# Kernel optimization log

Hardware: AMD Instinct MI355X
Metric: run time of the kernel (lower is better)

The kernel has to match this reference:

```python
import jax, jax.numpy as jnp
import numpy as np

DIM, NH, NKV, HD = 1024, 16, 16, 64
ROPE_BASE, TRAIN_LEN, YARN_MAX = 10000.0, 1024, 4096
GROUP = 64
EPS = 1e-05


def ternary_ste(w):
    # bf16 group-wise ternary quantization with straight-through estimator
    wb = w.astype(jnp.bfloat16)
    wg = wb.reshape(-1, GROUP)
    scale = jnp.clip(jnp.mean(jnp.abs(wg), axis=-1, keepdims=True), 1e-08, None)
    q = jnp.clip(jnp.round(wg / scale), -1, 1)
    deq = (q * scale).reshape(wb.shape)
    return wb + jax.lax.stop_gradient(deq - wb)


def rmsnorm(x):
    return x * jax.lax.rsqrt(jnp.mean(x * x, axis=-1, keepdims=True) + EPS)


def rope_tables(seqlen, dtype):
    rd = HD  # rope_dims=0 -> full head_dim
    ar = np.arange(0, rd, 2, dtype=np.float32)
    inv_freq = 1.0 / ROPE_BASE ** (ar / rd)
    scale = TRAIN_LEN / YARN_MAX
    ramp = np.clip((ar / rd - 0.25) / 0.75, 0.0, 1.0)
    inv_freq = inv_freq / (ramp * (1.0 / scale - 1.0) + 1.0)
    freqs = np.arange(seqlen, dtype=np.float32)[:, None] * inv_freq[None, :]
    cos = jnp.asarray(np.cos(freqs), dtype)[None, :, None, :]  # [1,S,1,HD/2]
    sin = jnp.asarray(np.sin(freqs), dtype)[None, :, None, :]
    return cos, sin


def apply_rotary(x, cos, sin):
    half = x.shape[-1] // 2
    x1, x2 = x[..., :half], x[..., half:]
    return jnp.concatenate([x1 * cos + x2 * sin, -x1 * sin + x2 * cos], axis=-1)


def causal_attn(q, k, v):
    # q,k,v: [B,S,H,d]; softmax scale 1/sqrt(d)
    d = q.shape[-1]
    S = q.shape[1]
    s = jnp.einsum('bqhd,bkhd->bhqk', q, k) * (1.0 / jnp.sqrt(jnp.asarray(d, q.dtype)))
    mask = jnp.tril(jnp.ones((S, S), bool))
    s = jnp.where(mask[None, None], s, -jnp.inf)
    p = jax.nn.softmax(s, axis=-1)
    return jnp.einsum('bhqk,bkhd->bqhd', p, v)


def tversky_proj(x, features, prototypes, theta, alpha, beta):
    # x: [B,S,D] -> [B,S,D]
    x_f = jnp.einsum('bsd,fd->bsf', x, features)          # [B,S,16]
    p_f = ternary_ste(prototypes).astype(features.dtype) @ features.T  # [D,16]
    x_s = jax.nn.sigmoid(x_f * 5.0)
    p_s = jax.nn.sigmoid(p_f * 5.0)
    x_a = x_f * x_s
    p_a = p_f * p_s
    return (jnp.abs(theta) * jnp.einsum('bsf,of->bso', x_a, p_a)
            - jnp.abs(alpha) * jnp.einsum('bsf,of->bso', x_a, 1.0 - p_s)
            - jnp.abs(beta) * jnp.einsum('bsf,of->bso', 1.0 - x_s, p_a))


def setup_inputs() -> dict:
    key = jax.random.key(0)
    ks = jax.random.split(key, 8)
    B, S = 2, 2048
    x = jax.random.normal(ks[0], (B, S, DIM), jnp.float32)
    w_qkv = jax.random.normal(ks[1], (NH * HD + 2 * NKV * HD, DIM), jnp.float32) * 0.02
    features = jax.random.uniform(ks[2], (16, DIM), jnp.float32, -0.02, 0.02)
    prototypes = jax.random.uniform(ks[3], (DIM, DIM), jnp.float32, -0.02, 0.02)
    theta = jnp.asarray(1.0, jnp.float32)
    alpha = jnp.asarray(0.5, jnp.float32)
    beta = jnp.asarray(0.5, jnp.float32)
    q_gain = jnp.full((NH,), 1.0, jnp.float32)
    diff_lambda = jnp.full((NH,), 0.5, jnp.float32)
    return {"x": x, "w_qkv": w_qkv, "features": features, "prototypes": prototypes,
            "theta": theta, "alpha": alpha, "beta": beta,
            "q_gain": q_gain, "diff_lambda": diff_lambda}


def reference(x, w_qkv, features, prototypes, theta, alpha, beta, q_gain, diff_lambda):
    B, S, D = x.shape
    w_t = ternary_ste(w_qkv).astype(x.dtype)
    qkv = x @ w_t.T
    q_out = qkv[..., :NH * HD]
    k_out = qkv[..., NH * HD:NH * HD + NKV * HD]
    v_out = qkv[..., NH * HD + NKV * HD:]
    q = rmsnorm(q_out.reshape(B, S, NH, HD))
    k = rmsnorm(k_out.reshape(B, S, NKV, HD))
    v = v_out.reshape(B, S, NKV, HD)
    cos, sin = rope_tables(S, q.dtype)
    q = apply_rotary(q, cos, sin)
    k = apply_rotary(k, cos, sin)
    q = q * q_gain.astype(q.dtype)[None, None, :, None]
    half = HD // 2
    y1 = causal_attn(q[..., :half], k[..., :half], v[..., :half])
    y2 = causal_attn(q[..., half:], k[..., half:], v[..., half:])
    lam = diff_lambda.astype(y1.dtype)[None, None, :, None]
    y = jnp.concatenate([y1 - lam * y2, y1 + lam * y2], axis=-1).reshape(B, S, D)
    return tversky_proj(y, features, prototypes, theta, alpha, beta)
```

## Files before the change

### kernel.cpp

```cpp
#include <hip/hip_runtime.h>
#include <hip/hip_bf16.h>
#include <math.h>

#define DIM   1024
#define NHEAD 16
#define SLEN  2048
#define BATCH 2
#define NROWS (BATCH*SLEN)
#define QKV_N 3072

typedef __attribute__((ext_vector_type(8))) short short8v;
typedef __attribute__((ext_vector_type(4))) short short4v;
typedef __attribute__((ext_vector_type(4))) float f32x4;
typedef __attribute__((ext_vector_type(4))) unsigned int u32x4;

__device__ __forceinline__ unsigned short rne16(float f) {
  unsigned u = __float_as_uint(f);
  u += 0x7FFFu + ((u >> 16) & 1u);
  return (unsigned short)(u >> 16);
}
__device__ __forceinline__ float rnef(float f) {
  unsigned u = __float_as_uint(f);
  u += 0x7FFFu + ((u >> 16) & 1u);
  return __uint_as_float(u & 0xFFFF0000u);
}
__device__ __forceinline__ unsigned pk2(float a, float b) {
  unsigned r;
  asm("v_cvt_pk_bf16_f32 %0, %1, %2" : "=v"(r) : "v"(a), "v"(b));
  return r;
}

__device__ __forceinline__ void gld16(const unsigned short* g, unsigned short* l) {
  __builtin_amdgcn_global_load_lds(
      (const __attribute__((address_space(1))) unsigned int*)g,
      (__attribute__((address_space(3))) unsigned int*)l, 16, 0, 0);
}

__global__ void __launch_bounds__(256) k_prep(
    const float* __restrict__ w_qkv, const float* __restrict__ protos,
    const float* __restrict__ x, const float* __restrict__ F,
    unsigned short* __restrict__ Wb, float* __restrict__ PT,
    unsigned short* __restrict__ Xhi, unsigned short* __restrict__ Xlo,
    float* __restrict__ cosT, float* __restrict__ sinT,
    float* __restrict__ FS, float* __restrict__ FD) {
  const int blk = blockIdx.x, tid = threadIdx.x;
  if (blk < 4096) {
    const bool isw = (blk < 3072);
    const int idx = (isw ? blk * 256 + tid : (blk - 3072) * 256 + tid) * 4;
    const float* src = isw ? w_qkv : protos;
    float4 v = *(const float4*)(src + idx);
    float b0 = rnef(v.x), b1 = rnef(v.y), b2 = rnef(v.z), b3 = rnef(v.w);
    float a0 = fabsf(b0), a1 = fabsf(b1), a2 = fabsf(b2), a3 = fabsf(b3);
    #pragma unroll
    for (int off = 8; off >= 1; off >>= 1) {
      a0 += __shfl_xor(a0, off); a1 += __shfl_xor(a1, off);
      a2 += __shfl_xor(a2, off); a3 += __shfl_xor(a3, off);
    }
    float s = (a0 + a2) + (a1 + a3);
    float scale = fmaxf(rnef(s * (1.0f / 64.0f)), 1e-8f);
    auto tern = [&](float wb) -> float {
      float q = fminf(1.0f, fmaxf(-1.0f, rintf(rnef(wb / scale))));
      float deq = rnef(q * scale);
      float d = rnef(deq - wb);
      return wb + d;
    };
    if (isw) {
      short4v o;
      o[0] = (short)rne16(tern(b0)); o[1] = (short)rne16(tern(b1));
      o[2] = (short)rne16(tern(b2)); o[3] = (short)rne16(tern(b3));
      *(short4v*)(Wb + idx) = o;
    } else {
      float4 o = {rnef(tern(b0)), rnef(tern(b1)), rnef(tern(b2)), rnef(tern(b3))};
      *(float4*)(PT + idx) = o;
    }
  } else if (blk < 8192) {
    int idx = (blk - 4096) * 256 + tid;
    float4 v = *(const float4*)(x + (size_t)idx * 4);
    short4v hi, lo;
    float h0 = rnef(v.x); hi[0] = (short)rne16(v.x); lo[0] = (short)rne16(v.x - h0);
    float h1 = rnef(v.y); hi[1] = (short)rne16(v.y); lo[1] = (short)rne16(v.y - h1);
    float h2 = rnef(v.z); hi[2] = (short)rne16(v.z); lo[2] = (short)rne16(v.z - h2);
    float h3 = rnef(v.w); hi[3] = (short)rne16(v.w); lo[3] = (short)rne16(v.w - h3);
    *(short4v*)(Xhi + (size_t)idx * 4) = hi;
    *(short4v*)(Xlo + (size_t)idx * 4) = lo;
  } else if (blk < 8448) {
    int idx = (blk - 8192) * 256 + tid;
    int s = idx >> 5, j = idx & 31;
    double inv  = 1.0 / pow(10000.0, (double)(2 * j) / 64.0);
    double ramp = ((double)(2 * j) / 64.0 - 0.25) / 0.75;
    ramp = ramp < 0.0 ? 0.0 : (ramp > 1.0 ? 1.0 : ramp);
    inv /= (ramp * 3.0 + 1.0);
    float freq = (float)s * (float)inv;
    cosT[idx] = (float)cos((double)freq);
    sinT[idx] = (float)sin((double)freq);
  } else {
    int idx = (blk - 8448) * 256 + tid;
    int f = idx >> 9, hd = idx & 511;
    int h = hd >> 5, d = hd & 31;
    float a = F[f * 1024 + h * 64 + d];
    float b = F[f * 1024 + h * 64 + 32 + d];
    FS[idx] = a + b;
    FD[idx] = b - a;
  }
}

#define FEN() asm volatile("" ::: "memory")
#define SB()  do { FEN(); __builtin_amdgcn_s_barrier(); FEN(); } while (0)
#define WL()  do { asm volatile("s_waitcnt lgkmcnt(0)" ::: "memory"); \
                   __builtin_amdgcn_sched_barrier(0); } while (0)
#define WVN(n) asm volatile("s_waitcnt vmcnt(" #n ")" ::: "memory")

__global__ void __launch_bounds__(512, 2) k_gemm4(
    const unsigned short* __restrict__ Xhi, const unsigned short* __restrict__ Xlo,
    const unsigned short* __restrict__ Wb, float* __restrict__ C) {
  __shared__ unsigned char lds[114688];
  const int t = threadIdx.x;
  const int lane = t & 63;
  const int qL = lane & 15, quad = lane >> 4;
  const int wid = t >> 6;
  const int wm = wid >> 2, wn = wid & 3;
  const int bid = blockIdx.x;
  const int swz = (bid & 7) * 32 + (bid >> 3);
  const int by = swz >> 4, bx = swz & 15;
  const int bm = by * 256, bn = bx * 192;
  const int inner = qL * 64 + ((quad * 16) ^ ((qL & 8) << 2));
  int rj[3], cj[3];
  #pragma unroll
  for (int j = 0; j < 3; ++j) {
    int L = j * 8192 + t * 16;
    int Lp = L ^ (((L >> 9) & 1) << 5);
    int st = Lp >> 10;
    rj[j] = (st >> 1) * 16 + ((Lp >> 6) & 15);
    cj[j] = (st & 1) * 32 + ((Lp & 63) >> 1);
  }
  unsigned char* AHI = lds;
  unsigned char* ALO = lds + 32768;
  unsigned char* BB  = lds + 65536;

  auto STA = [&](const unsigned short* __restrict__ pan, unsigned char* reg,
                 int kc, int h) {
    unsigned char* lb = reg + h * 16384 + (t >> 6) * 1024;
    #pragma unroll
    for (int j = 0; j < 2; ++j) {
      int rr = bm + ((rj[j] >> 6) * 128) + h * 64 + (rj[j] & 63);
      gld16(pan + (size_t)rr * 1024 + kc + cj[j], (unsigned short*)(lb + j * 8192));
    }
  };
  auto STB = [&](int kc, int buf) {
    unsigned char* lb = BB + buf * 24576 + (t >> 6) * 1024;
    #pragma unroll
    for (int j = 0; j < 3; ++j)
      gld16(Wb + (size_t)(bn + rj[j]) * 1024 + kc + cj[j],
            (unsigned short*)(lb + j * 8192));
  };

  short8v aF[4][2], bF[3][2];
  f32x4 acc[2][4][3];
  const f32x4 zz = {0.f, 0.f, 0.f, 0.f};
  #pragma unroll
  for (int q_ = 0; q_ < 2; ++q_)
    #pragma unroll
    for (int m_ = 0; m_ < 4; ++m_)
      #pragma unroll
      for (int n_ = 0; n_ < 3; ++n_) acc[q_][m_][n_] = zz;

  auto RA = [&](unsigned char* reg, int qm_) {
    #pragma unroll
    for (int mi = 0; mi < 4; ++mi)
      #pragma unroll
      for (int ks = 0; ks < 2; ++ks)
        aF[mi][ks] = *(const short8v*)(reg + qm_ * 16384 +
                                       ((((wm * 4 + mi) << 1) + ks) << 10) + inner);
  };
  auto RB = [&](int buf) {
    #pragma unroll
    for (int ni = 0; ni < 3; ++ni)
      #pragma unroll
      for (int ks = 0; ks < 2; ++ks)
        bF[ni][ks] = *(const short8v*)(BB + buf * 24576 +
                                       ((((wn * 3 + ni) << 1) + ks) << 10) + inner);
  };
  auto MM = [&](int qm_) {
    __builtin_amdgcn_s_setprio(1);
    #pragma unroll
    for (int ks = 0; ks < 2; ++ks)
      #pragma unroll
      for (int mi = 0; mi < 4; ++mi)
        #pragma unroll
        for (int ni = 0; ni < 3; ++ni)
          acc[qm_][mi][ni] = __builtin_amdgcn_mfma_f32_16x16x32_bf16(
              aF[mi][ks], bF[ni][ks], acc[qm_][mi][ni], 0, 0, 0);
    __builtin_amdgcn_s_setprio(0);
  };

  STB(0, 0); STA(Xhi, AHI, 0, 0); STA(Xhi, AHI, 0, 1); STA(Xlo, ALO, 0, 0);
  WVN(4);
  SB();

  #pragma unroll 1
  for (int i = 0; i < 16; ++i) {
    const int kc = i * 64, kn = kc + 64;
    const bool nl = (i < 15);
    const int cb = i & 1, nb = cb ^ 1;
    RA(AHI, 0); RB(cb); STA(Xlo, ALO, kc, 1);
    SB(); WL(); MM(0);
    WVN(4);
    SB();
    RA(AHI, 1);
    if (nl) { STB(kn, nb); STA(Xhi, AHI, kn, 0); }
    SB(); WL(); MM(1);
    if (nl) { WVN(7); } else { WVN(2); }
    SB();
    RA(ALO, 0);
    if (nl) STA(Xhi, AHI, kn, 1);
    SB(); WL(); MM(0);
    if (nl) { WVN(7); } else { WVN(0); }
    SB();
    RA(ALO, 1);
    if (nl) STA(Xlo, ALO, kn, 0);
    SB(); WL(); MM(1);
    if (nl) WVN(4);
    SB();
  }

  #pragma unroll
  for (int qm_ = 0; qm_ < 2; ++qm_)
    #pragma unroll
    for (int mi = 0; mi < 4; ++mi) {
      const int row0 = bm + wm * 128 + qm_ * 64 + mi * 16 + quad * 4;
      #pragma unroll
      for (int ni = 0; ni < 3; ++ni) {
        const int col = bn + wn * 48 + ni * 16 + qL;
        #pragma unroll
        for (int r = 0; r < 4; ++r)
          C[(size_t)(row0 + r) * QKV_N + col] = acc[qm_][mi][ni][r];
      }
    }
}

__device__ __forceinline__ float dot4(float4 a, float4 b) {
  return fmaf(a.x, b.x, fmaf(a.y, b.y, fmaf(a.z, b.z, a.w * b.w)));
}
__global__ void __launch_bounds__(256) k_mid(const float* __restrict__ QKV,
    const float* __restrict__ cosT, const float* __restrict__ sinT,
    const float* __restrict__ q_gain,
    unsigned short* __restrict__ QB16, unsigned short* __restrict__ KB16,
    unsigned short* __restrict__ VT16,
    const float* __restrict__ PT, const float* __restrict__ F,
    const float* __restrict__ thp, const float* __restrict__ alp,
    const float* __restrict__ bep,
    float* __restrict__ A1T, float* __restrict__ A2T) {
  __shared__ short Vt[64][34];
  const int blk = blockIdx.x, t = threadIdx.x;
  if (blk < 8192) {
    int gid = blk * 256 + t;
    int l = gid & 63;
    int w = gid >> 6;
    int r = w >> 3;
    int u = (w & 7) * 4 + (l >> 4);
    int isk = u >> 4, h = u & 15;
    int d0 = (l & 15) * 4;
    float4 xv = *(const float4*)(QKV + (size_t)r * 3072 + isk * 1024 + h * 64 + d0);
    float s0 = xv.x * xv.x, s1 = xv.y * xv.y;
    float s2 = xv.z * xv.z, s3 = xv.w * xv.w;
    #pragma unroll
    for (int off = 8; off >= 1; off >>= 1) {
      s0 += __shfl_xor(s0, off); s1 += __shfl_xor(s1, off);
      s2 += __shfl_xor(s2, off); s3 += __shfl_xor(s3, off);
    }
    float ss = (s0 + s2) + (s1 + s3);
    float inv = rsqrtf(ss * (1.0f / 64.0f) + 1e-5f);
    float xn0 = xv.x * inv, xn1 = xv.y * inv;
    float xn2 = xv.z * inv, xn3 = xv.w * inv;
    int s = r & (SLEN - 1);
    int b = r >> 11;
    int j4 = (l & 7) * 4;
    float4 c4 = *(const float4*)(cosT + s * 32 + j4);
    float4 n4 = *(const float4*)(sinT + s * 32 + j4);
    float ot0 = __shfl_xor(xn0, 8), ot1 = __shfl_xor(xn1, 8);
    float ot2 = __shfl_xor(xn2, 8), ot3 = __shfl_xor(xn3, 8);
    const bool hi = (l & 8) != 0;
    float o0 = hi ? fmaf(xn0, c4.x, -ot0 * n4.x) : fmaf(xn0, c4.x, ot0 * n4.x);
    float o1 = hi ? fmaf(xn1, c4.y, -ot1 * n4.y) : fmaf(xn1, c4.y, ot1 * n4.y);
    float o2 = hi ? fmaf(xn2, c4.z, -ot2 * n4.z) : fmaf(xn2, c4.z, ot2 * n4.z);
    float o3 = hi ? fmaf(xn3, c4.w, -ot3 * n4.w) : fmaf(xn3, c4.w, ot3 * n4.w);
    int hh = h + (hi ? 16 : 0);
    size_t addr = (((size_t)(b * 32 + hh) * SLEN) + s) * 32 + (l & 7) * 4;
    short4v o;
    if (!isk) {
      const float FOLD = 0.17677669529663687f * 1.4426950408889634f;
      float g = q_gain[h];
      o[0] = (short)rne16(o0 * g * FOLD); o[1] = (short)rne16(o1 * g * FOLD);
      o[2] = (short)rne16(o2 * g * FOLD); o[3] = (short)rne16(o3 * g * FOLD);
      *(short4v*)(QB16 + addr) = o;
    } else {
      o[0] = (short)rne16(o0); o[1] = (short)rne16(o1);
      o[2] = (short)rne16(o2); o[3] = (short)rne16(o3);
      *(short4v*)(KB16 + addr) = o;
    }
  } else if (blk < 10240) {
    int i = blk - 8192;
    const int s0 = (i & 31) * 64, hh = (i >> 5) & 31, b = i >> 10;
    const int vcb = 2048 + (hh & 15) * 64 + (hh >> 4) * 32;
    {
      int row = t >> 2, dpart = (t & 3) * 8;
      const float* p = QKV + (size_t)(b * SLEN + s0 + row) * 3072 + vcb + dpart;
      float4 a = *(const float4*)p;
      float4 bq = *(const float4*)(p + 4);
      Vt[row][dpart + 0] = (short)rne16(a.x);  Vt[row][dpart + 1] = (short)rne16(a.y);
      Vt[row][dpart + 2] = (short)rne16(a.z);  Vt[row][dpart + 3] = (short)rne16(a.w);
      Vt[row][dpart + 4] = (short)rne16(bq.x); Vt[row][dpart + 5] = (short)rne16(bq.y);
      Vt[row][dpart + 6] = (short)rne16(bq.z); Vt[row][dpart + 7] = (short)rne16(bq.w);
    }
    __syncthreads();
    {
      int d = t >> 3, j = t & 7;
      short8v v;
      #pragma unroll
      for (int k = 0; k < 8; ++k) v[k] = Vt[j * 8 + k][d];
      const int m = j & 3;
      const int cb = s0 + ((j >> 2) << 5);
      const int p0 = ((m & 1) << 4) + ((m >> 1) << 2);
      unsigned short* basep =
          VT16 + (((size_t)(b * 32 + hh) * 32) + d) * SLEN + cb + p0;
      short4v lo = __builtin_shufflevector(v, v, 0, 1, 2, 3);
      short4v hi = __builtin_shufflevector(v, v, 4, 5, 6, 7);
      *(short4v*)basep = lo;
      *(short4v*)(basep + 8) = hi;
    }
  } else {
    const int w = t >> 6, lane = t & 63;
    const int o = (blk - 10240) * 4 + w;
    const float* pr = PT + (size_t)o * 1024;
    float4 p0 = *(const float4*)(pr + lane * 4);
    float4 p1 = *(const float4*)(pr + 256 + lane * 4);
    float4 p2 = *(const float4*)(pr + 512 + lane * 4);
    float4 p3 = *(const float4*)(pr + 768 + lane * 4);
    float acc[16];
    #pragma unroll
    for (int f = 0; f < 16; ++f) {
      const float* fr = F + (size_t)f * 1024;
      float4 f0 = *(const float4*)(fr + lane * 4);
      float4 f1 = *(const float4*)(fr + 256 + lane * 4);
      float4 f2 = *(const float4*)(fr + 512 + lane * 4);
      float4 f3 = *(const float4*)(fr + 768 + lane * 4);
      acc[f] = dot4(p0, f0) + dot4(p1, f1) + dot4(p2, f2) + dot4(p3, f3);
    }
    #pragma unroll
    for (int f = 0; f < 16; ++f) {
      #pragma unroll
      for (int off = 32; off >= 1; off >>= 1) acc[f] += __shfl_xor(acc[f], off);
    }
    if (lane == 0) {
      float th = fabsf(*thp), al = fabsf(*alp), be = fabsf(*bep);
      #pragma unroll
      for (int f = 0; f < 16; ++f) {
        float pf = acc[f];
        float ps = 1.0f / (1.0f + expf(-5.0f * pf));
        float pa = pf * ps;
        A1T[f * 1024 + o] = th * pa - al * (1.0f - ps);
        A2T[f * 1024 + o] = -be * pa;
      }
    }
  }
}

__global__ void __launch_bounds__(256, 6) k_attn(
    const unsigned short* __restrict__ QB16,
    const unsigned short* __restrict__ KB16,
    const unsigned short* __restrict__ VT16,
    float* __restrict__ OH) {
  __shared__ unsigned char kv[2][4096];
  const int wid = threadIdx.x >> 6;
  const int lane = threadIdx.x & 63;
  const int qL = lane & 15, quad = lane >> 4;
  const int bk = blockIdx.x;
  const int combo = bk & 63;
  const int ii = bk >> 6, qd = ii >> 2, rr = ii & 3;
  const int G = (qd & 1) ? (rr + ((qd & 2) << 1)) : (15 - rr - ((qd & 2) << 1));
  const int qbw = 4 * G + wid;
  const int cmax = 4 * G + 3;
  const int b = combo >> 5, hh = combo & 31;
  const int q0 = qbw * 32;

  const unsigned short* QB = QB16 + (size_t)(b * 32 + hh) * SLEN * 32;
  const unsigned short* KB = KB16 + (size_t)(b * 32 + hh) * SLEN * 32;
  const unsigned short* VT = VT16 + (size_t)(b * 32 + hh) * 32 * SLEN;

  const short8v qf0 = *(const short8v*)(QB + (size_t)(q0 + qL) * 32 + quad * 8);
  const short8v qf1 = *(const short8v*)(QB + (size_t)(q0 + 16 + qL) * 32 + quad * 8);
  const f32x4 zz = {0.f, 0.f, 0.f, 0.f};
  f32x4 a00 = zz, a01 = zz, a10 = zz, a11 = zz;
  float l0 = 0.f, l1 = 0.f;

  const unsigned short* sbase = (wid < 2)
      ? KB + (size_t)(wid * 16 + qL) * 32 + quad * 8
      : VT + (size_t)((wid - 2) * 16 + qL) * 2048 + quad * 8;
  const int sstep = (wid < 2) ? 1024 : 32;
  unsigned short* d0 = (unsigned short*)(&kv[0][0] + wid * 1024);
  unsigned short* d1 = (unsigned short*)(&kv[1][0] + wid * 1024);

  gld16(sbase, d0);
  WVN(0);
  SB();

  #pragma unroll 1
  for (int c = 0; c <= cmax; ++c) {
    const unsigned char* kb = &kv[c & 1][0];
    if (c < cmax) gld16(sbase + (size_t)(c + 1) * sstep, (c & 1) ? d0 : d1);
    if (c <= qbw) {
      short8v kf0 = *(const short8v*)(kb + lane * 16);
      short8v kf1 = *(const short8v*)(kb + 1024 + lane * 16);
      short8v vf0 = *(const short8v*)(kb + 2048 + lane * 16);
      short8v vf1 = *(const short8v*)(kb + 3072 + lane * 16);
      if (c < qbw) {
        f32x4 s00 = __builtin_amdgcn_mfma_f32_16x16x32_bf16(kf0, qf0, zz, 0, 0, 0);
        f32x4 s01 = __builtin_amdgcn_mfma_f32_16x16x32_bf16(kf1, qf0, zz, 0, 0, 0);
        f32x4 s10 = __builtin_amdgcn_mfma_f32_16x16x32_bf16(kf0, qf1, zz, 0, 0, 0);
        f32x4 s11 = __builtin_amdgcn_mfma_f32_16x16x32_bf16(kf1, qf1, zz, 0, 0, 0);
        float p00[4], p01[4], p10[4], p11[4];
        #pragma unroll
        for (int r = 0; r < 4; ++r) {
          p00[r] = __builtin_amdgcn_exp2f(s00[r]);
          p01[r] = __builtin_amdgcn_exp2f(s01[r]);
          p10[r] = __builtin_amdgcn_exp2f(s10[r]);
          p11[r] = __builtin_amdgcn_exp2f(s11[r]);
        }
        l0 += (p00[0] + p00[1] + p00[2] + p00[3]) + (p01[0] + p01[1] + p01[2] + p01[3]);
        l1 += (p10[0] + p10[1] + p10[2] + p10[3]) + (p11[0] + p11[1] + p11[2] + p11[3]);
        u32x4 up0 = {pk2(p00[0], p00[1]), pk2(p00[2], p00[3]),
                     pk2(p01[0], p01[1]), pk2(p01[2], p01[3])};
        u32x4 up1 = {pk2(p10[0], p10[1]), pk2(p10[2], p10[3]),
                     pk2(p11[0], p11[1]), pk2(p11[2], p11[3])};
        short8v pf0 = __builtin_bit_cast(short8v, up0);
        short8v pf1 = __builtin_bit_cast(short8v, up1);
        a00 = __builtin_amdgcn_mfma_f32_16x16x32_bf16(vf0, pf0, a00, 0, 0, 0);
        a01 = __builtin_amdgcn_mfma_f32_16x16x32_bf16(vf1, pf0, a01, 0, 0, 0);
        a10 = __builtin_amdgcn_mfma_f32_16x16x32_bf16(vf0, pf1, a10, 0, 0, 0);
        a11 = __builtin_amdgcn_mfma_f32_16x16x32_bf16(vf1, pf1, a11, 0, 0, 0);
      } else {
        f32x4 s00 = __builtin_amdgcn_mfma_f32_16x16x32_bf16(kf0, qf0, zz, 0, 0, 0);
        f32x4 s10 = __builtin_amdgcn_mfma_f32_16x16x32_bf16(kf0, qf1, zz, 0, 0, 0);
        f32x4 s11 = __builtin_amdgcn_mfma_f32_16x16x32_bf16(kf1, qf1, zz, 0, 0, 0);
        float p00[4], p10[4], p11[4];
        #pragma unroll
        for (int r = 0; r < 4; ++r) {
          bool v = (4 * quad + r) <= qL;
          p00[r] = v ? __builtin_amdgcn_exp2f(s00[r]) : 0.f;
          p10[r] = __builtin_amdgcn_exp2f(s10[r]);
          p11[r] = v ? __builtin_amdgcn_exp2f(s11[r]) : 0.f;
        }
        l0 += (p00[0] + p00[1] + p00[2] + p00[3]);
        l1 += (p10[0] + p10[1] + p10[2] + p10[3]) + (p11[0] + p11[1] + p11[2] + p11[3]);
        u32x4 up0 = {pk2(p00[0], p00[1]), pk2(p00[2], p00[3]), 0u, 0u};
        u32x4 up1 = {pk2(p10[0], p10[1]), pk2(p10[2], p10[3]),
                     pk2(p11[0], p11[1]), pk2(p11[2], p11[3])};
        short8v pf0 = __builtin_bit_cast(short8v, up0);
        short8v pf1 = __builtin_bit_cast(short8v, up1);
        a00 = __builtin_amdgcn_mfma_f32_16x16x32_bf16(vf0, pf0, a00, 0, 0, 0);
        a01 = __builtin_amdgcn_mfma_f32_16x16x32_bf16(vf1, pf0, a01, 0, 0, 0);
        a10 = __builtin_amdgcn_mfma_f32_16x16x32_bf16(vf0, pf1, a10, 0, 0, 0);
        a11 = __builtin_amdgcn_mfma_f32_16x16x32_bf16(vf1, pf1, a11, 0, 0, 0);
      }
    }
    if (c < cmax) WVN(0);
    SB();
  }

  l0 += __shfl_xor(l0, 16); l0 += __shfl_xor(l0, 32);
  l1 += __shfl_xor(l1, 16); l1 += __shfl_xor(l1, 32);
  const float inv0 = 1.0f / l0, inv1 = 1.0f / l1;
  float* ob0 = OH + (((size_t)(b * SLEN + q0 + qL) * 32) + hh) * 32 + (quad << 2);
  float* ob1 = OH + (((size_t)(b * SLEN + q0 + 16 + qL) * 32) + hh) * 32 + (quad << 2);
  *(float4*)ob0        = (float4){a00[0] * inv0, a00[1] * inv0, a00[2] * inv0, a00[3] * inv0};
  *(float4*)(ob0 + 16) = (float4){a01[0] * inv0, a01[1] * inv0, a01[2] * inv0, a01[3] * inv0};
  *(float4*)ob1        = (float4){a10[0] * inv1, a10[1] * inv1, a10[2] * inv1, a10[3] * inv1};
  *(float4*)(ob1 + 16) = (float4){a11[0] * inv1, a11[1] * inv1, a11[2] * inv1, a11[3] * inv1};
}

__global__ void __launch_bounds__(256) k_tail(const float* __restrict__ OH,
    const float* __restrict__ dl, const float* __restrict__ FS,
    const float* __restrict__ FD, const float* __restrict__ A1T,
    const float* __restrict__ A2T, float* __restrict__ out) {
  __shared__ float XAs[8][16];
  __shared__ float XS1s[8][16];
  const int t = threadIdx.x;
  const int w = t >> 6, lane = t & 63;
  const int rbase = blockIdx.x * 8;
  {
    const float lam0 = dl[lane >> 3];
    const float lam1 = dl[8 + (lane >> 3)];
    const float* oh0 = OH + (size_t)(rbase + w * 2) * 1024;
    float4 y1a0 = *(const float4*)(oh0 + lane * 4);
    float4 y1b0 = *(const float4*)(oh0 + 256 + lane * 4);
    float4 y2a0 = *(const float4*)(oh0 + 512 + lane * 4);
    float4 y2b0 = *(const float4*)(oh0 + 768 + lane * 4);
    float4 y1a1 = *(const float4*)(oh0 + 1024 + lane * 4);
    float4 y1b1 = *(const float4*)(oh0 + 1280 + lane * 4);
    float4 y2a1 = *(const float4*)(oh0 + 1536 + lane * 4);
    float4 y2b1 = *(const float4*)(oh0 + 1792 + lane * 4);
    y2a0.x *= lam0; y2a0.y *= lam0; y2a0.z *= lam0; y2a0.w *= lam0;
    y2b0.x *= lam1; y2b0.y *= lam1; y2b0.z *= lam1; y2b0.w *= lam1;
    y2a1.x *= lam0; y2a1.y *= lam0; y2a1.z *= lam0; y2a1.w *= lam0;
    y2b1.x *= lam1; y2b1.y *= lam1; y2b1.z *= lam1; y2b1.w *= lam1;
    float acc0[16], acc1[16];
    #pragma unroll
    for (int f = 0; f < 16; ++f) {
      float4 sa = *(const float4*)(FS + f * 512 + lane * 4);
      float4 sb = *(const float4*)(FS + f * 512 + 256 + lane * 4);
      float4 da = *(const float4*)(FD + f * 512 + lane * 4);
      float4 db = *(const float4*)(FD + f * 512 + 256 + lane * 4);
      acc0[f] = dot4(y1a0, sa) + dot4(y1b0, sb) + dot4(y2a0, da) + dot4(y2b0, db);
      acc1[f] = dot4(y1a1, sa) + dot4(y1b1, sb) + dot4(y2a1, da) + dot4(y2b1, db);
    }
    #pragma unroll
    for (int f = 0; f < 16; ++f) {
      #pragma unroll
      for (int off = 32; off >= 1; off >>= 1) {
        acc0[f] += __shfl_xor(acc0[f], off);
        acc1[f] += __shfl_xor(acc1[f], off);
      }
    }
    if (lane == 0) {
      #pragma unroll
      for (int f = 0; f < 16; ++f) {
        float xf = acc0[f];
        float xs = 1.0f / (1.0f + expf(-5.0f * xf));
        XAs[w * 2][f] = xf * xs;
        XS1s[w * 2][f] = 1.0f - xs;
        float xg = acc1[f];
        float xt = 1.0f / (1.0f + expf(-5.0f * xg));
        XAs[w * 2 + 1][f] = xg * xt;
        XS1s[w * 2 + 1][f] = 1.0f - xt;
      }
    }
  }
  __syncthreads();
  {
    float4 acc[8];
    #pragma unroll
    for (int rr = 0; rr < 8; ++rr) acc[rr] = (float4){0.f, 0.f, 0.f, 0.f};
    #pragma unroll
    for (int f = 0; f < 16; ++f) {
      float4 a1 = *(const float4*)(A1T + f * 1024 + t * 4);
      float4 a2 = *(const float4*)(A2T + f * 1024 + t * 4);
      #pragma unroll
      for (int rr = 0; rr < 8; ++rr) {
        float xa = XAs[rr][f], x1 = XS1s[rr][f];
        acc[rr].x = fmaf(xa, a1.x, fmaf(x1, a2.x, acc[rr].x));
        acc[rr].y = fmaf(xa, a1.y, fmaf(x1, a2.y, acc[rr].y));
        acc[rr].z = fmaf(xa, a1.z, fmaf(x1, a2.z, acc[rr].z));
        acc[rr].w = fmaf(xa, a1.w, fmaf(x1, a2.w, acc[rr].w));
      }
    }
    #pragma unroll
    for (int rr = 0; rr < 8; ++rr)
      *(float4*)(out + (size_t)(rbase + rr) * 1024 + t * 4) = acc[rr];
  }
}

extern "C" void kernel_launch(void* const* d_in, const int* in_sizes, int n_in,
                              void* d_out, int out_size, void* d_ws, size_t ws_size,
                              hipStream_t stream) {
  const float* x      = (const float*)d_in[0];
  const float* w_qkv  = (const float*)d_in[1];
  const float* feats  = (const float*)d_in[2];
  const float* protos = (const float*)d_in[3];
  const float* theta  = (const float*)d_in[4];
  const float* alpha  = (const float*)d_in[5];
  const float* beta   = (const float*)d_in[6];
  const float* q_gain = (const float*)d_in[7];
  const float* dlam   = (const float*)d_in[8];
  float* out = (float*)d_out;
  float* ws  = (float*)d_ws;

  float* QKV = ws;
  float* OH  = QKV + 12582912;
  float* COS = OH  + 4194304;
  float* SIN = COS + 65536;
  float* PT  = SIN + 65536;
  float* A1T = PT  + 1048576;
  float* A2T = A1T + 16384;
  float* XA  = A2T + 16384;
  float* XS1 = XA  + 65536;
  unsigned short* QB16 = (unsigned short*)(XS1 + 65536);
  unsigned short* KB16 = QB16 + 4194304;
  unsigned short* VT16 = KB16 + 4194304;
  unsigned short* Wb   = VT16 + 4194304;
  unsigned short* Xhi  = Wb   + 3145728;
  unsigned short* Xlo  = Xhi  + 4194304;
  float* FS = (float*)(Xlo + 4194304);
  float* FD = FS + 8192;

  k_prep<<<8480, 256, 0, stream>>>(w_qkv, protos, x, feats, Wb, PT,
                                   Xhi, Xlo, COS, SIN, FS, FD);
  k_gemm4<<<256, 512, 0, stream>>>(Xhi, Xlo, Wb, QKV);
  k_mid<<<10496, 256, 0, stream>>>(QKV, COS, SIN, q_gain, QB16, KB16, VT16,
                                   PT, feats, theta, alpha, beta, A1T, A2T);
  k_attn<<<1024, 256, 0, stream>>>(QB16, KB16, VT16, OH);
  k_tail<<<512, 256, 0, stream>>>(OH, dlam, FS, FD, A1T, A2T, out);
}
```

Baseline: 220.1 us.

## Fuse RMSNorm, RoPE and bf16 packing of Q/K/V into the QKV GEMM epilogue

```diff
diff --git a/kernel.cpp b/kernel.cpp
--- a/kernel.cpp
+++ b/kernel.cpp
@@ -112,7 +112,11 @@
 
 __global__ void __launch_bounds__(512, 2) k_gemm4(
     const unsigned short* __restrict__ Xhi, const unsigned short* __restrict__ Xlo,
-    const unsigned short* __restrict__ Wb, float* __restrict__ C) {
+    const unsigned short* __restrict__ Wb,
+    const float* __restrict__ cosT, const float* __restrict__ sinT,
+    const float* __restrict__ q_gain,
+    unsigned short* __restrict__ QB16, unsigned short* __restrict__ KB16,
+    unsigned short* __restrict__ VT16) {
   __shared__ unsigned char lds[114688];
   const int t = threadIdx.x;
   const int lane = t & 63;
@@ -223,144 +227,142 @@
     SB();
   }
 
-  #pragma unroll
-  for (int qm_ = 0; qm_ < 2; ++qm_)
-    #pragma unroll
-    for (int mi = 0; mi < 4; ++mi) {
-      const int row0 = bm + wm * 128 + qm_ * 64 + mi * 16 + quad * 4;
+  float* S = (float*)lds;
+  const int bb = bm >> 11;
+  const int lg = t & 15;
+  const int g16 = t >> 4;
+  const int gch0 = bn >> 6;
+
+  auto EPI = [&](const f32x4 (&ap)[4][3], int p) {
+    #pragma unroll
+    for (int mi = 0; mi < 4; ++mi)
       #pragma unroll
       for (int ni = 0; ni < 3; ++ni) {
-        const int col = bn + wn * 48 + ni * 16 + qL;
+        const int sr = wm * 64 + mi * 16 + quad * 4;
+        const int colL = wn * 48 + ni * 16 + qL;
         #pragma unroll
         for (int r = 0; r < 4; ++r)
-          C[(size_t)(row0 + r) * QKV_N + col] = acc[qm_][mi][ni][r];
+          S[(sr + r) * 196 + colL] = ap[mi][ni][r];
       }
-    }
+    SB();
+    #pragma unroll 1
+    for (int u = g16; u < 384; u += 32) {
+      const int chunk = u >> 7, sr = u & 127;
+      const int gch = gch0 + chunk;
+      if (gch < 32) {
+        float4 xv = *(const float4*)&S[sr * 196 + chunk * 64 + lg * 4];
+        float s0 = xv.x * xv.x, s1 = xv.y * xv.y;
+        float s2 = xv.z * xv.z, s3 = xv.w * xv.w;
+        #pragma unroll
+        for (int off = 8; off >= 1; off >>= 1) {
+          s0 += __shfl_xor(s0, off); s1 += __shfl_xor(s1, off);
+          s2 += __shfl_xor(s2, off); s3 += __shfl_xor(s3, off);
+        }
+        float ss = (s0 + s2) + (s1 + s3);
+        float inv = rsqrtf(ss * (1.0f / 64.0f) + 1e-5f);
+        float xn0 = xv.x * inv, xn1 = xv.y * inv;
+        float xn2 = xv.z * inv, xn3 = xv.w * inv;
+        const int s_glob = bm + ((sr >> 6) << 7) + p * 64 + (sr & 63);
+        const int srow = s_glob & (SLEN - 1);
+        const int j4 = (lg & 7) * 4;
+        float4 c4 = *(const float4*)(cosT + srow * 32 + j4);
+        float4 n4 = *(const float4*)(sinT + srow * 32 + j4);
+        float ot0 = __shfl_xor(xn0, 8), ot1 = __shfl_xor(xn1, 8);
+        float ot2 = __shfl_xor(xn2, 8), ot3 = __shfl_xor(xn3, 8);
+        const bool hi = (lg & 8) != 0;
+        float o0 = hi ? fmaf(xn0, c4.x, -ot0 * n4.x) : fmaf(xn0, c4.x, ot0 * n4.x);
+        float o1 = hi ? fmaf(xn1, c4.y, -ot1 * n4.y) : fmaf(xn1, c4.y, ot1 * n4.y);
+        float o2 = hi ? fmaf(xn2, c4.z, -ot2 * n4.z) : fmaf(xn2, c4.z, ot2 * n4.z);
+        float o3 = hi ? fmaf(xn3, c4.w, -ot3 * n4.w) : fmaf(xn3, c4.w, ot3 * n4.w);
+        const int h = gch & 15;
+        const int hh = h + (hi ? 16 : 0);
+        size_t addr = (((size_t)(bb * 32 + hh) * SLEN) + srow) * 32 + j4;
+        short4v o;
+        if (gch < 16) {
+          const float FOLD = 0.17677669529663687f * 1.4426950408889634f;
+          float gq = q_gain[h];
+          o[0] = (short)rne16(o0 * gq * FOLD); o[1] = (short)rne16(o1 * gq * FOLD);
+          o[2] = (short)rne16(o2 * gq * FOLD); o[3] = (short)rne16(o3 * gq * FOLD);
+          *(short4v*)(QB16 + addr) = o;
+        } else {
+          o[0] = (short)rne16(o0); o[1] = (short)rne16(o1);
+          o[2] = (short)rne16(o2); o[3] = (short)rne16(o3);
+          *(short4v*)(KB16 + addr) = o;
+        }
+      }
+    }
+    const int wid8 = t >> 6;
+    const int cl = t & 63;
+    #pragma unroll 1
+    for (int c3 = 0; c3 < 3; ++c3) {
+      const int gch = gch0 + c3;
+      if (gch >= 32) {
+        const int hv = gch - 32;
+        const int hh = (cl >= 32) ? hv + 16 : hv;
+        const int dpl = cl & 31;
+        unsigned short* vrow = VT16 + (((size_t)(bb * 32 + hh) * 32) + dpl) * SLEN;
+        #pragma unroll
+        for (int k4 = 0; k4 < 4; ++k4) {
+          const int sr = wid8 * 16 + k4 * 4;
+          const int s_glob = bm + ((sr >> 6) << 7) + p * 64 + (sr & 63);
+          const int srow = s_glob & (SLEN - 1);
+          const int c32 = srow & ~31, kc = srow & 31;
+          const int p0 = 8 * ((kc & 15) >> 2) + 4 * (kc >> 4);
+          short4v o;
+          o[0] = (short)rne16(S[(sr + 0) * 196 + c3 * 64 + cl]);
+          o[1] = (short)rne16(S[(sr + 1) * 196 + c3 * 64 + cl]);
+          o[2] = (short)rne16(S[(sr + 2) * 196 + c3 * 64 + cl]);
+          o[3] = (short)rne16(S[(sr + 3) * 196 + c3 * 64 + cl]);
+          *(short4v*)(vrow + c32 + p0) = o;
+        }
+      }
+    }
+    SB();
+  };
+  EPI(acc[0], 0);
+  EPI(acc[1], 1);
 }
 
 __device__ __forceinline__ float dot4(float4 a, float4 b) {
   return fmaf(a.x, b.x, fmaf(a.y, b.y, fmaf(a.z, b.z, a.w * b.w)));
 }
-__global__ void __launch_bounds__(256) k_mid(const float* __restrict__ QKV,
-    const float* __restrict__ cosT, const float* __restrict__ sinT,
-    const float* __restrict__ q_gain,
-    unsigned short* __restrict__ QB16, unsigned short* __restrict__ KB16,
-    unsigned short* __restrict__ VT16,
+__global__ void __launch_bounds__(256) k_mid(
     const float* __restrict__ PT, const float* __restrict__ F,
     const float* __restrict__ thp, const float* __restrict__ alp,
     const float* __restrict__ bep,
     float* __restrict__ A1T, float* __restrict__ A2T) {
-  __shared__ short Vt[64][34];
-  const int blk = blockIdx.x, t = threadIdx.x;
-  if (blk < 8192) {
-    int gid = blk * 256 + t;
-    int l = gid & 63;
-    int w = gid >> 6;
-    int r = w >> 3;
-    int u = (w & 7) * 4 + (l >> 4);
-    int isk = u >> 4, h = u & 15;
-    int d0 = (l & 15) * 4;
-    float4 xv = *(const float4*)(QKV + (size_t)r * 3072 + isk * 1024 + h * 64 + d0);
-    float s0 = xv.x * xv.x, s1 = xv.y * xv.y;
-    float s2 = xv.z * xv.z, s3 = xv.w * xv.w;
-    #pragma unroll
-    for (int off = 8; off >= 1; off >>= 1) {
-      s0 += __shfl_xor(s0, off); s1 += __shfl_xor(s1, off);
-      s2 += __shfl_xor(s2, off); s3 += __shfl_xor(s3, off);
-    }
-    float ss = (s0 + s2) + (s1 + s3);
-    float inv = rsqrtf(ss * (1.0f / 64.0f) + 1e-5f);
-    float xn0 = xv.x * inv, xn1 = xv.y * inv;
-    float xn2 = xv.z * inv, xn3 = xv.w * inv;
-    int s = r & (SLEN - 1);
-    int b = r >> 11;
-    int j4 = (l & 7) * 4;
-    float4 c4 = *(const float4*)(cosT + s * 32 + j4);
-    float4 n4 = *(const float4*)(sinT + s * 32 + j4);
-    float ot0 = __shfl_xor(xn0, 8), ot1 = __shfl_xor(xn1, 8);
-    float ot2 = __shfl_xor(xn2, 8), ot3 = __shfl_xor(xn3, 8);
-    const bool hi = (l & 8) != 0;
-    float o0 = hi ? fmaf(xn0, c4.x, -ot0 * n4.x) : fmaf(xn0, c4.x, ot0 * n4.x);
-    float o1 = hi ? fmaf(xn1, c4.y, -ot1 * n4.y) : fmaf(xn1, c4.y, ot1 * n4.y);
-    float o2 = hi ? fmaf(xn2, c4.z, -ot2 * n4.z) : fmaf(xn2, c4.z, ot2 * n4.z);
-    float o3 = hi ? fmaf(xn3, c4.w, -ot3 * n4.w) : fmaf(xn3, c4.w, ot3 * n4.w);
-    int hh = h + (hi ? 16 : 0);
-    size_t addr = (((size_t)(b * 32 + hh) * SLEN) + s) * 32 + (l & 7) * 4;
-    short4v o;
-    if (!isk) {
-      const float FOLD = 0.17677669529663687f * 1.4426950408889634f;
-      float g = q_gain[h];
-      o[0] = (short)rne16(o0 * g * FOLD); o[1] = (short)rne16(o1 * g * FOLD);
-      o[2] = (short)rne16(o2 * g * FOLD); o[3] = (short)rne16(o3 * g * FOLD);
-      *(short4v*)(QB16 + addr) = o;
-    } else {
-      o[0] = (short)rne16(o0); o[1] = (short)rne16(o1);
-      o[2] = (short)rne16(o2); o[3] = (short)rne16(o3);
-      *(short4v*)(KB16 + addr) = o;
-    }
-  } else if (blk < 10240) {
-    int i = blk - 8192;
-    const int s0 = (i & 31) * 64, hh = (i >> 5) & 31, b = i >> 10;
-    const int vcb = 2048 + (hh & 15) * 64 + (hh >> 4) * 32;
-    {
-      int row = t >> 2, dpart = (t & 3) * 8;
-      const float* p = QKV + (size_t)(b * SLEN + s0 + row) * 3072 + vcb + dpart;
-      float4 a = *(const float4*)p;
-      float4 bq = *(const float4*)(p + 4);
-      Vt[row][dpart + 0] = (short)rne16(a.x);  Vt[row][dpart + 1] = (short)rne16(a.y);
-      Vt[row][dpart + 2] = (short)rne16(a.z);  Vt[row][dpart + 3] = (short)rne16(a.w);
-      Vt[row][dpart + 4] = (short)rne16(bq.x); Vt[row][dpart + 5] = (short)rne16(bq.y);
-      Vt[row][dpart + 6] = (short)rne16(bq.z); Vt[row][dpart + 7] = (short)rne16(bq.w);
-    }
-    __syncthreads();
-    {
-      int d = t >> 3, j = t & 7;
-      short8v v;
-      #pragma unroll
-      for (int k = 0; k < 8; ++k) v[k] = Vt[j * 8 + k][d];
-      const int m = j & 3;
-      const int cb = s0 + ((j >> 2) << 5);
-      const int p0 = ((m & 1) << 4) + ((m >> 1) << 2);
-      unsigned short* basep =
-          VT16 + (((size_t)(b * 32 + hh) * 32) + d) * SLEN + cb + p0;
-      short4v lo = __builtin_shufflevector(v, v, 0, 1, 2, 3);
-      short4v hi = __builtin_shufflevector(v, v, 4, 5, 6, 7);
-      *(short4v*)basep = lo;
-      *(short4v*)(basep + 8) = hi;
-    }
-  } else {
-    const int w = t >> 6, lane = t & 63;
-    const int o = (blk - 10240) * 4 + w;
-    const float* pr = PT + (size_t)o * 1024;
-    float4 p0 = *(const float4*)(pr + lane * 4);
-    float4 p1 = *(const float4*)(pr + 256 + lane * 4);
-    float4 p2 = *(const float4*)(pr + 512 + lane * 4);
-    float4 p3 = *(const float4*)(pr + 768 + lane * 4);
-    float acc[16];
+  const int t = threadIdx.x;
+  const int w = t >> 6, lane = t & 63;
+  const int o = blockIdx.x * 4 + w;
+  const float* pr = PT + (size_t)o * 1024;
+  float4 p0 = *(const float4*)(pr + lane * 4);
+  float4 p1 = *(const float4*)(pr + 256 + lane * 4);
+  float4 p2 = *(const float4*)(pr + 512 + lane * 4);
+  float4 p3 = *(const float4*)(pr + 768 + lane * 4);
+  float acc[16];
+  #pragma unroll
+  for (int f = 0; f < 16; ++f) {
+    const float* fr = F + (size_t)f * 1024;
+    float4 f0 = *(const float4*)(fr + lane * 4);
+    float4 f1 = *(const float4*)(fr + 256 + lane * 4);
+    float4 f2 = *(const float4*)(fr + 512 + lane * 4);
+    float4 f3 = *(const float4*)(fr + 768 + lane * 4);
+    acc[f] = dot4(p0, f0) + dot4(p1, f1) + dot4(p2, f2) + dot4(p3, f3);
+  }
+  #pragma unroll
+  for (int f = 0; f < 16; ++f) {
+    #pragma unroll
+    for (int off = 32; off >= 1; off >>= 1) acc[f] += __shfl_xor(acc[f], off);
+  }
+  if (lane == 0) {
+    float th = fabsf(*thp), al = fabsf(*alp), be = fabsf(*bep);
     #pragma unroll
     for (int f = 0; f < 16; ++f) {
-      const float* fr = F + (size_t)f * 1024;
-      float4 f0 = *(const float4*)(fr + lane * 4);
-      float4 f1 = *(const float4*)(fr + 256 + lane * 4);
-      float4 f2 = *(const float4*)(fr + 512 + lane * 4);
-      float4 f3 = *(const float4*)(fr + 768 + lane * 4);
-      acc[f] = dot4(p0, f0) + dot4(p1, f1) + dot4(p2, f2) + dot4(p3, f3);
-    }
-    #pragma unroll
-    for (int f = 0; f < 16; ++f) {
-      #pragma unroll
-      for (int off = 32; off >= 1; off >>= 1) acc[f] += __shfl_xor(acc[f], off);
-    }
-    if (lane == 0) {
-      float th = fabsf(*thp), al = fabsf(*alp), be = fabsf(*bep);
-      #pragma unroll
-      for (int f = 0; f < 16; ++f) {
-        float pf = acc[f];
-        float ps = 1.0f / (1.0f + expf(-5.0f * pf));
-        float pa = pf * ps;
-        A1T[f * 1024 + o] = th * pa - al * (1.0f - ps);
-        A2T[f * 1024 + o] = -be * pa;
-      }
+      float pf = acc[f];
+      float ps = 1.0f / (1.0f + expf(-5.0f * pf));
+      float pa = pf * ps;
+      A1T[f * 1024 + o] = th * pa - al * (1.0f - ps);
+      A2T[f * 1024 + o] = -be * pa;
     }
   }
 }
@@ -574,16 +576,13 @@
   float* out = (float*)d_out;
   float* ws  = (float*)d_ws;
 
-  float* QKV = ws;
-  float* OH  = QKV + 12582912;
+  float* OH  = ws;
   float* COS = OH  + 4194304;
   float* SIN = COS + 65536;
   float* PT  = SIN + 65536;
   float* A1T = PT  + 1048576;
   float* A2T = A1T + 16384;
-  float* XA  = A2T + 16384;
-  float* XS1 = XA  + 65536;
-  unsigned short* QB16 = (unsigned short*)(XS1 + 65536);
+  unsigned short* QB16 = (unsigned short*)(A2T + 16384);
   unsigned short* KB16 = QB16 + 4194304;
   unsigned short* VT16 = KB16 + 4194304;
   unsigned short* Wb   = VT16 + 4194304;
@@ -594,9 +593,9 @@
 
   k_prep<<<8480, 256, 0, stream>>>(w_qkv, protos, x, feats, Wb, PT,
                                    Xhi, Xlo, COS, SIN, FS, FD);
-  k_gemm4<<<256, 512, 0, stream>>>(Xhi, Xlo, Wb, QKV);
-  k_mid<<<10496, 256, 0, stream>>>(QKV, COS, SIN, q_gain, QB16, KB16, VT16,
-                                   PT, feats, theta, alpha, beta, A1T, A2T);
+  k_gemm4<<<256, 512, 0, stream>>>(Xhi, Xlo, Wb, COS, SIN, q_gain,
+                                   QB16, KB16, VT16);
+  k_mid<<<256, 256, 0, stream>>>(PT, feats, theta, alpha, beta, A1T, A2T);
   k_attn<<<1024, 256, 0, stream>>>(QB16, KB16, VT16, OH);
   k_tail<<<512, 256, 0, stream>>>(OH, dlam, FS, FD, A1T, A2T, out);
 }
```

Measured after the change: 219.5 us. About the same (-0.3%).
